# Optimization experiments

Measured on AMD Instinct MI355X. Metric: run time of the kernel, lower is better.

Reference implementation:

```python
import jax, jax.numpy as jnp
import numpy as np

SR = 16000
MAX_Q = 2.0
MIN_D, MAX_D = 0.1, 2.0
MIN_W = 2.0 * np.pi * 20.0 / SR  # 2*pi*20/sr, lowest cutoff in rad/sample
MIN_Q = 0.1
B, T = 32, 65536


def map_logspace(x, lo, hi):
    # log-spaced interpolation: x in [0,1] -> [lo, hi]
    return lo * (hi / lo) ** x


def segment_average(params, seg_ids, num_segments):
    # average params over each onset-delimited segment, broadcast back to [B,T,4]
    def one(p, s):
        sums = jax.ops.segment_sum(p, s, num_segments=num_segments)
        cnt = jax.ops.segment_sum(jnp.ones(s.shape, p.dtype), s, num_segments=num_segments)
        avg = sums / jnp.maximum(cnt, 1.0)[:, None]
        return avg[s]
    return jax.vmap(one)(params, seg_ids)


def pluck_comb(f0, mu, x):
    # Mathematically identical to the scatter-built dense (B,T,D) FIR in the
    # original: y[b,t] = x[b,t] - (1-alfa)*x[b, t-(z+1)] - alfa*x[b, t-(z+2)]
    # (lag k corresponds to coefficient slot k-1; out-of-range lags are zero).
    Tx = x.shape[1]
    p = f0 * mu                       # fractional pluck position in samples
    z = jnp.floor(p)
    alfa = p - z
    zi = z.astype(jnp.int32)
    t = jnp.arange(Tx, dtype=jnp.int32)[None, :]

    def lag(idx):
        g = jnp.take_along_axis(x, jnp.clip(idx, 0, Tx - 1), axis=1)
        return jnp.where(idx >= 0, g, jnp.zeros((), x.dtype))

    return x - (1.0 - alfa) * lag(t - (zi + 1)) - alfa * lag(t - (zi + 2))


def tv_lp_biquad(x, w_mod, q_mod):
    # Time-varying RBJ low-pass biquad, transposed direct-form II, coefficients
    # recomputed per sample from w_mod,q_mod in (0,1).
    w = map_logspace(w_mod, MIN_W, jnp.pi)     # cutoff rad/sample in [min_w, pi]
    q = map_logspace(q_mod, MIN_Q, MAX_Q)      # resonance in [0.1, max_q]
    cw, sw = jnp.cos(w), jnp.sin(w)
    alpha = sw / (2.0 * q)
    a0 = 1.0 + alpha
    b0 = (1.0 - cw) / (2.0 * a0)
    b1 = (1.0 - cw) / a0
    b2 = b0
    a1 = (-2.0 * cw) / a0
    a2 = (1.0 - alpha) / a0

    xs = tuple(jnp.swapaxes(a, 0, 1) for a in (x, b0, b1, b2, a1, a2))  # [T,B]

    def step(carry, inp):
        s1, s2 = carry
        xt, b0t, b1t, b2t, a1t, a2t = inp
        y = b0t * xt + s1
        s1n = b1t * xt - a1t * y + s2
        s2n = b2t * xt - a2t * y
        return (s1n, s2n), y

    Bx = x.shape[0]
    init = (jnp.zeros((Bx,), x.dtype), jnp.zeros((Bx,), x.dtype))
    _, y = jax.lax.scan(step, init, xs)
    return jnp.swapaxes(y, 0, 1)


def _forward(f0, x, params, onsets):
    Tx = x.shape[1]
    # segment ids: cumulative count of onsets along time
    seg_ids = jnp.cumsum(onsets.astype(jnp.int32), axis=1)
    params = segment_average(params, seg_ids, Tx + 1)
    distance = map_logspace(jax.nn.sigmoid(params[..., 0]), MIN_D, MAX_D)
    w_mod = jax.nn.sigmoid(params[..., 1])
    q_mod = jax.nn.sigmoid(params[..., 2])
    mu = jax.nn.sigmoid(params[..., 3])
    xd = x * distance
    xc = pluck_comb(f0, mu, xd)
    return tv_lp_biquad(xc, w_mod, q_mod)


def setup_inputs() -> dict:
    key = jax.random.key(0)
    k1, k2, k3, k4 = jax.random.split(key, 4)
    # f0 is a fundamental period in samples (80-160 Hz at sr=16k)
    f0 = 100.0 + 100.0 * jax.random.uniform(k1, (B, T), jnp.float32)
    x = jax.random.normal(k2, (B, T), jnp.float32)
    params = jax.random.normal(k3, (B, T, 4), jnp.float32)
    onsets = (jax.random.uniform(k4, (B, T)) < 1e-3).astype(jnp.int32)  # sparse note onsets
    return {"f0": f0, "input": x, "params": params, "onsets": onsets}


def reference(f0, input, params, onsets):
    return _forward(f0, input, params, onsets)
```

## Files before the change

### kernel.cpp

```cpp
#include <hip/hip_runtime.h>
#include <cstdint>


namespace {
constexpr int B = 32;
constexpr int T = 65536;
constexpr int MAXSEG = 2048;
constexpr int SB = 2048;
constexpr int HALO = 256;
constexpr int PARTS = T / SB;
constexpr int NB = B * PARTS;

constexpr float MIN_W_C  = 0.00785398163397448279f;
constexpr float LOG2_400 = 8.64385618977472436f;
constexpr float LOG2_20  = 4.32192809488736235f;

__device__ __forceinline__ float sigmoid_precise(float v) {
  return 1.0f / (1.0f + expf(-v));
}
__device__ __forceinline__ int pad16(int i) { return i + (i >> 4); }
}

__global__ void __launch_bounds__(1024) k_segids(
    const int* __restrict__ onsets, unsigned short* __restrict__ seg_ids,
    int* __restrict__ onsetPos, int* __restrict__ nseg) {
  __shared__ int wcnt[16];
  int b = blockIdx.x, tid = threadIdx.x;
  int w = tid >> 6, lane = tid & 63;
  int rb = b * T;
  int sp = w * 4096;
  const int4* po = (const int4*)(onsets + rb + sp);
  int run = 0;
#pragma unroll 4
  for (int it = 0; it < 16; ++it) {
    int4 v = po[it * 64 + lane];
    run += (v.x != 0) + (v.y != 0) + (v.z != 0) + (v.w != 0);
  }
  for (int off = 32; off; off >>= 1) run += __shfl_down(run, off);
  if (lane == 0) wcnt[w] = run;
  __syncthreads();
  int base = 0, tot = 0;
  for (int i = 0; i < 16; ++i) { int c = wcnt[i]; tot += c; if (i < w) base += c; }
  if (tid == 0) nseg[b] = tot;
  unsigned long long bm = (1ull << lane) - 1ull;
  int runp = base;
  for (int it = 0; it < 16; ++it) {
    int tb = sp + it * 256;
    int o0 = onsets[rb + tb + lane];
    int o1 = onsets[rb + tb + 64 + lane];
    int o2 = onsets[rb + tb + 128 + lane];
    int o3 = onsets[rb + tb + 192 + lane];
    int os[4] = {o0 != 0, o1 != 0, o2 != 0, o3 != 0};
#pragma unroll
    for (int j = 0; j < 4; ++j) {
      int t = tb + j * 64 + lane;
      unsigned long long m = __ballot(os[j]);
      int sid = runp + __popcll(m & bm) + os[j];
      seg_ids[rb + t] = (unsigned short)min(sid, MAXSEG - 1);
      if (os[j] && sid <= MAXSEG) onsetPos[b * MAXSEG + sid - 1] = t;
      runp += __popcll(m);
    }
  }
}

__global__ void k_segavg(const float* __restrict__ params, const int* __restrict__ onsetPos,
                         const int* __restrict__ nseg, float4* __restrict__ segc,
                         float* __restrict__ segd) {
  __shared__ float part[4][4];
  int b = blockIdx.x >> 6;
  int s0 = blockIdx.x & 63;
  int tid = threadIdx.x;
  int n = nseg[b];
  const float4* pp = (const float4*)params;
  for (int s = s0; s <= n; s += 64) {
    int start = (s == 0) ? 0 : onsetPos[b * MAXSEG + min(s, MAXSEG) - 1];
    int end   = (s == n) ? T : onsetPos[b * MAXSEG + min(s, MAXSEG - 1)];
    float a0 = 0.f, a1 = 0.f, a2 = 0.f, a3 = 0.f;
    for (int t = start + tid; t < end; t += 256) {
      float4 pv = pp[b * T + t];
      a0 += pv.x; a1 += pv.y; a2 += pv.z; a3 += pv.w;
    }
    for (int off = 32; off; off >>= 1) {
      a0 += __shfl_down(a0, off); a1 += __shfl_down(a1, off);
      a2 += __shfl_down(a2, off); a3 += __shfl_down(a3, off);
    }
    if ((tid & 63) == 0) {
      int w = tid >> 6;
      part[w][0] = a0; part[w][1] = a1; part[w][2] = a2; part[w][3] = a3;
    }
    __syncthreads();
    if (tid == 0) {
      float t0 = 0.f, t1 = 0.f, t2 = 0.f, t3 = 0.f;
      for (int w = 0; w < 4; ++w) {
        t0 += part[w][0]; t1 += part[w][1]; t2 += part[w][2]; t3 += part[w][3];
      }
      float inv = 1.0f / (float)max(end - start, 1);
      float av0 = t0 * inv, av1 = t1 * inv, av2 = t2 * inv, av3 = t3 * inv;
      float dist = 0.1f * exp2f(sigmoid_precise(av0) * LOG2_20);
      float wv   = MIN_W_C * exp2f(sigmoid_precise(av1) * LOG2_400);
      float qv   = 0.1f * exp2f(sigmoid_precise(av2) * LOG2_20);
      float mu   = sigmoid_precise(av3);
      float sw = sinf(wv), cw = cosf(wv);
      float alpha = sw / (2.0f * qv);
      float a0c = 1.0f + alpha;
      float b0 = (1.0f - cw) / (2.0f * a0c);
      float na1 = 2.0f * cw / a0c;
      float na2 = (alpha - 1.0f) / a0c;
      int sl = min(s, MAXSEG - 1);
      segc[b * MAXSEG + sl] = make_float4(mu, b0, na1, na2);
      segd[b * MAXSEG + sl] = dist;
    }
    __syncthreads();
  }
}

__global__ void __launch_bounds__(256) k_compose(
    const float* __restrict__ f0, const float* __restrict__ x,
    const unsigned short* __restrict__ seg, const float4* __restrict__ segc,
    const float* __restrict__ segd, float* __restrict__ p0g,
    float* __restrict__ aggP) {
  __shared__ float s_xd[2448];
  __shared__ float wagg[4][6];
  int tid = threadIdx.x;
  int blk = blockIdx.x;
  int b = blk >> 5, part = blk & (PARTS - 1);
  int rb = b * T, rs = b * MAXSEG, bs = part * SB;

  for (int j = tid; j < SB + HALO; j += 256) {
    int tr = bs - HALO + j;
    float v = 0.f;
    if (tr >= 0) {
      int s = (int)seg[rb + tr];
      v = x[rb + tr] * segd[rs + s];
    }
    s_xd[pad16(j)] = v;
  }
  __syncthreads();

  int lane = tid & 63, w = tid >> 6;
  int t0l = tid * 8;
  const float4* f4 = (const float4*)(f0 + rb + bs + t0l);
  const uint4* sg4 = (const uint4*)(seg + rb + bs + t0l);
  uint4 sv = sg4[0];
  unsigned sw_[4] = {sv.x, sv.y, sv.z, sv.w};
  float p0c[8];
  float A00 = 1.f, A01 = 0.f, A10 = 0.f, A11 = 1.f, d0 = 0.f, d1 = 0.f;
#pragma unroll
  for (int k = 0; k < 2; ++k) {
    float4 fv = f4[k];
    float fs[4] = {fv.x, fv.y, fv.z, fv.w};
#pragma unroll
    for (int q = 0; q < 4; ++q) {
      int idx = k * 4 + q;
      int li = t0l + idx;
      int s = (int)((sw_[idx >> 1] >> (16 * (idx & 1))) & 0xFFFFu);
      float4 sc = segc[rs + s];
      float p = fs[q] * sc.x;
      float z = floorf(p);
      float alfa = p - z;
      int zi = min((int)z, HALO - 8);
      int i1 = li - zi - 1 + HALO;
      float xl1 = s_xd[pad16(i1)];
      float xl2 = s_xd[pad16(i1 - 1)];
      float xc = s_xd[pad16(li + HALO)] - (1.f - alfa) * xl1 - alfa * xl2;
      float p0 = sc.y * xc;
      p0c[idx] = p0;
      float na1 = sc.z, na2 = sc.w;
      float c0v = p0 * (2.f + na1);
      float c1v = p0 * (1.f + na2);
      float nA00 = fmaf(na1, A00, A10);
      float nA01 = fmaf(na1, A01, A11);
      float nd0  = fmaf(na1, d0, d1 + c0v);
      float nA10 = na2 * A00;
      float nA11 = na2 * A01;
      float nd1  = fmaf(na2, d0, c1v);
      A00 = nA00; A01 = nA01; A10 = nA10; A11 = nA11; d0 = nd0; d1 = nd1;
    }
  }
  float4* pp4 = (float4*)(p0g + rb + bs + t0l);
  pp4[0] = make_float4(p0c[0], p0c[1], p0c[2], p0c[3]);
  pp4[1] = make_float4(p0c[4], p0c[5], p0c[6], p0c[7]);
#pragma unroll
  for (int off = 1; off < 64; off <<= 1) {
    float R00 = __shfl_down(A00, off), R01 = __shfl_down(A01, off);
    float R10 = __shfl_down(A10, off), R11 = __shfl_down(A11, off);
    float Rd0 = __shfl_down(d0, off),  Rd1 = __shfl_down(d1, off);
    float n00 = fmaf(R00, A00, R01 * A10);
    float n01 = fmaf(R00, A01, R01 * A11);
    float n10 = fmaf(R10, A00, R11 * A10);
    float n11 = fmaf(R10, A01, R11 * A11);
    float nd0 = fmaf(R00, d0, fmaf(R01, d1, Rd0));
    float nd1 = fmaf(R10, d0, fmaf(R11, d1, Rd1));
    A00 = n00; A01 = n01; A10 = n10; A11 = n11; d0 = nd0; d1 = nd1;
  }
  if (lane == 0) {
    wagg[w][0] = A00; wagg[w][1] = A01; wagg[w][2] = A10;
    wagg[w][3] = A11; wagg[w][4] = d0;  wagg[w][5] = d1;
  }
  __syncthreads();
  if (tid == 0) {
    float G00 = wagg[0][0], G01 = wagg[0][1], G10 = wagg[0][2];
    float G11 = wagg[0][3], Gd0 = wagg[0][4], Gd1 = wagg[0][5];
    for (int i = 1; i < 4; ++i) {
      float W00 = wagg[i][0], W01 = wagg[i][1], W10 = wagg[i][2];
      float W11 = wagg[i][3], Wd0 = wagg[i][4], Wd1 = wagg[i][5];
      float n00 = fmaf(W00, G00, W01 * G10);
      float n01 = fmaf(W00, G01, W01 * G11);
      float n10 = fmaf(W10, G00, W11 * G10);
      float n11 = fmaf(W10, G01, W11 * G11);
      float nd0 = fmaf(W00, Gd0, fmaf(W01, Gd1, Wd0));
      float nd1 = fmaf(W10, Gd0, fmaf(W11, Gd1, Wd1));
      G00 = n00; G01 = n01; G10 = n10; G11 = n11; Gd0 = nd0; Gd1 = nd1;
    }
    float* gp = aggP + blk * 6;
    gp[0] = G00; gp[1] = G01; gp[2] = G10; gp[3] = G11; gp[4] = Gd0; gp[5] = Gd1;
  }
}

__global__ void __launch_bounds__(256) k_apply(
    const float* __restrict__ p0g, const unsigned short* __restrict__ seg,
    const float4* __restrict__ segc, const float* __restrict__ aggP,
    float* __restrict__ out) {
  __shared__ float wagg[4][6];
  __shared__ float rowpref[2];
  int tid = threadIdx.x;
  int blk = blockIdx.x;
  int b = blk >> 5, part = blk & (PARTS - 1);
  int rb = b * T, rs = b * MAXSEG, bs = part * SB;
  int lane = tid & 63, w = tid >> 6;
  int t0l = tid * 8;

  const float4* pp4 = (const float4*)(p0g + rb + bs + t0l);
  const uint4* sg4 = (const uint4*)(seg + rb + bs + t0l);
  uint4 sv = sg4[0];
  unsigned sw_[4] = {sv.x, sv.y, sv.z, sv.w};
  float p0c[8], na1c[8], na2c[8];
  float A00 = 1.f, A01 = 0.f, A10 = 0.f, A11 = 1.f, d0 = 0.f, d1 = 0.f;
#pragma unroll
  for (int k = 0; k < 2; ++k) {
    float4 pv = pp4[k];
    float ps[4] = {pv.x, pv.y, pv.z, pv.w};
#pragma unroll
    for (int q = 0; q < 4; ++q) {
      int idx = k * 4 + q;
      int s = (int)((sw_[idx >> 1] >> (16 * (idx & 1))) & 0xFFFFu);
      float4 sc = segc[rs + s];
      float p0 = ps[q];
      float na1 = sc.z, na2 = sc.w;
      p0c[idx] = p0; na1c[idx] = na1; na2c[idx] = na2;
      float c0v = p0 * (2.f + na1);
      float c1v = p0 * (1.f + na2);
      float nA00 = fmaf(na1, A00, A10);
      float nA01 = fmaf(na1, A01, A11);
      float nd0  = fmaf(na1, d0, d1 + c0v);
      float nA10 = na2 * A00;
      float nA11 = na2 * A01;
      float nd1  = fmaf(na2, d0, c1v);
      A00 = nA00; A01 = nA01; A10 = nA10; A11 = nA11; d0 = nd0; d1 = nd1;
    }
  }
#pragma unroll
  for (int off = 1; off < 64; off <<= 1) {
    float P00 = __shfl_up(A00, off), P01 = __shfl_up(A01, off);
    float P10 = __shfl_up(A10, off), P11 = __shfl_up(A11, off);
    float Pd0 = __shfl_up(d0, off),  Pd1 = __shfl_up(d1, off);
    if (lane >= off) {
      float nA00 = fmaf(A00, P00, A01 * P10);
      float nA01 = fmaf(A00, P01, A01 * P11);
      float nA10 = fmaf(A10, P00, A11 * P10);
      float nA11 = fmaf(A10, P01, A11 * P11);
      float nd0  = fmaf(A00, Pd0, fmaf(A01, Pd1, d0));
      float nd1  = fmaf(A10, Pd0, fmaf(A11, Pd1, d1));
      A00 = nA00; A01 = nA01; A10 = nA10; A11 = nA11; d0 = nd0; d1 = nd1;
    }
  }
  if (lane == 63) {
    wagg[w][0] = A00; wagg[w][1] = A01; wagg[w][2] = A10;
    wagg[w][3] = A11; wagg[w][4] = d0;  wagg[w][5] = d1;
  }
  if (tid == 0) {
    float R00 = 1.f, R01 = 0.f, R10 = 0.f, R11 = 1.f, Rd0 = 0.f, Rd1 = 0.f;
    int base = (blk - part) * 6;
    for (int j = 0; j < part; ++j) {
      const float* gp = aggP + base + j * 6;
      float W00 = gp[0], W01 = gp[1], W10 = gp[2], W11 = gp[3], Wd0 = gp[4], Wd1 = gp[5];
      float n00 = fmaf(W00, R00, W01 * R10);
      float n01 = fmaf(W00, R01, W01 * R11);
      float n10 = fmaf(W10, R00, W11 * R10);
      float n11 = fmaf(W10, R01, W11 * R11);
      float nd0 = fmaf(W00, Rd0, fmaf(W01, Rd1, Wd0));
      float nd1 = fmaf(W10, Rd0, fmaf(W11, Rd1, Wd1));
      R00 = n00; R01 = n01; R10 = n10; R11 = n11; Rd0 = nd0; Rd1 = nd1;
    }
    rowpref[0] = Rd0; rowpref[1] = Rd1;
  }
  __syncthreads();
  float E00 = __shfl_up(A00, 1), E01 = __shfl_up(A01, 1);
  float E10 = __shfl_up(A10, 1), E11 = __shfl_up(A11, 1);
  float Ed0 = __shfl_up(d0, 1),  Ed1 = __shfl_up(d1, 1);
  if (lane == 0) { E00 = 1.f; E01 = 0.f; E10 = 0.f; E11 = 1.f; Ed0 = 0.f; Ed1 = 0.f; }
  float P00 = 1.f, P01 = 0.f, P10 = 0.f, P11 = 1.f, Pd0 = 0.f, Pd1 = 0.f;
  for (int i = 0; i < w; ++i) {
    float W00 = wagg[i][0], W01 = wagg[i][1], W10 = wagg[i][2];
    float W11 = wagg[i][3], Wd0 = wagg[i][4], Wd1 = wagg[i][5];
    float n00 = fmaf(W00, P00, W01 * P10);
    float n01 = fmaf(W00, P01, W01 * P11);
    float n10 = fmaf(W10, P00, W11 * P10);
    float n11 = fmaf(W10, P01, W11 * P11);
    float nd0 = fmaf(W00, Pd0, fmaf(W01, Pd1, Wd0));
    float nd1 = fmaf(W10, Pd0, fmaf(W11, Pd1, Wd1));
    P00 = n00; P01 = n01; P10 = n10; P11 = n11; Pd0 = nd0; Pd1 = nd1;
  }
  float X00 = fmaf(E00, P00, E01 * P10);
  float X01 = fmaf(E00, P01, E01 * P11);
  float X10 = fmaf(E10, P00, E11 * P10);
  float X11 = fmaf(E10, P01, E11 * P11);
  float Xd0 = fmaf(E00, Pd0, fmaf(E01, Pd1, Ed0));
  float Xd1 = fmaf(E10, Pd0, fmaf(E11, Pd1, Ed1));
  float r0 = rowpref[0], r1 = rowpref[1];
  float s1 = fmaf(X00, r0, fmaf(X01, r1, Xd0));
  float s2 = fmaf(X10, r0, fmaf(X11, r1, Xd1));
  float4* o4 = (float4*)(out + rb + bs + t0l);
#pragma unroll
  for (int k = 0; k < 2; ++k) {
    float ys[4];
#pragma unroll
    for (int q = 0; q < 4; ++q) {
      int idx = k * 4 + q;
      float p0 = p0c[idx];
      float y = p0 + s1;
      ys[q] = y;
      float ns1 = fmaf(na1c[idx], y, fmaf(2.f, p0, s2));
      float ns2 = fmaf(na2c[idx], y, p0);
      s1 = ns1; s2 = ns2;
    }
    o4[k] = make_float4(ys[0], ys[1], ys[2], ys[3]);
  }
}

extern "C" void kernel_launch(void* const* d_in, const int* in_sizes, int n_in,
                              void* d_out, int out_size, void* d_ws, size_t ws_size,
                              hipStream_t stream) {
  const float* f0     = (const float*)d_in[0];
  const float* x      = (const float*)d_in[1];
  const float* params = (const float*)d_in[2];
  const int*   onsets = (const int*)d_in[3];
  float* out = (float*)d_out;

  char* w = (char*)d_ws;
  auto alloc = [&](size_t bytes) -> void* {
    void* p = (void*)w;
    w += (bytes + 255) & ~(size_t)255;
    return p;
  };
  unsigned short* seg_ids = (unsigned short*)alloc(sizeof(unsigned short) * B * T);
  int*    onsetPos = (int*)alloc(sizeof(int) * B * MAXSEG);
  int*    nseg     = (int*)alloc(sizeof(int) * B);
  float4* segc     = (float4*)alloc(sizeof(float4) * B * MAXSEG);
  float*  segd     = (float*)alloc(sizeof(float) * B * MAXSEG);
  float*  p0g      = (float*)alloc(sizeof(float) * B * T);
  float*  aggP     = (float*)alloc(sizeof(float) * 6 * NB);
  (void)in_sizes; (void)n_in; (void)out_size; (void)ws_size;

  k_segids <<<B, 1024, 0, stream>>>(onsets, seg_ids, onsetPos, nseg);
  k_segavg <<<B * 64, 256, 0, stream>>>(params, onsetPos, nseg, segc, segd);
  k_compose<<<NB, 256, 0, stream>>>(f0, x, seg_ids, segc, segd, p0g, aggP);
  k_apply  <<<NB, 256, 0, stream>>>(p0g, seg_ids, segc, aggP, out);
}
```

Measured before the change: 130.5 us.

## Split segment-id scan into count and scan kernels across more waves

Replaces the single per-batch 1024-thread segment-id kernel (32 blocks) with two kernels: a count kernel where each of 64 waves per batch row counts onsets in its span, and a scan kernel that computes exclusive prefixes across waves with shuffles before writing segment ids and onset positions. The aim is to spread the scan over 512 blocks so more of the GPU is busy in this stage. The cost is an extra kernel launch and a second read of the onsets array, and the scan loop now issues one scalar load per iteration instead of four.

```diff
diff --git a/kernel.cpp b/kernel.cpp
--- a/kernel.cpp
+++ b/kernel.cpp
@@ -6,6 +6,8 @@
 constexpr int B = 32;
 constexpr int T = 65536;
 constexpr int MAXSEG = 2048;
+constexpr int WV = 64;
+constexpr int SPAN = T / WV;
 constexpr int SB = 2048;
 constexpr int HALO = 256;
 constexpr int PARTS = T / SB;
@@ -21,45 +23,45 @@
 __device__ __forceinline__ int pad16(int i) { return i + (i >> 4); }
 }
 
-__global__ void __launch_bounds__(1024) k_segids(
-    const int* __restrict__ onsets, unsigned short* __restrict__ seg_ids,
-    int* __restrict__ onsetPos, int* __restrict__ nseg) {
-  __shared__ int wcnt[16];
-  int b = blockIdx.x, tid = threadIdx.x;
-  int w = tid >> 6, lane = tid & 63;
-  int rb = b * T;
-  int sp = w * 4096;
-  const int4* po = (const int4*)(onsets + rb + sp);
+__global__ void k_count(const int* __restrict__ onsets, int* __restrict__ cnt) {
+  int gw = (blockIdx.x * blockDim.x + threadIdx.x) >> 6;
+  int lane = threadIdx.x & 63;
+  int b = gw / WV, wv = gw % WV;
+  const int4* po = (const int4*)(onsets + b * T + wv * SPAN);
   int run = 0;
-#pragma unroll 4
-  for (int it = 0; it < 16; ++it) {
+  for (int it = 0; it < SPAN / 256; ++it) {
     int4 v = po[it * 64 + lane];
     run += (v.x != 0) + (v.y != 0) + (v.z != 0) + (v.w != 0);
   }
   for (int off = 32; off; off >>= 1) run += __shfl_down(run, off);
-  if (lane == 0) wcnt[w] = run;
-  __syncthreads();
-  int base = 0, tot = 0;
-  for (int i = 0; i < 16; ++i) { int c = wcnt[i]; tot += c; if (i < w) base += c; }
-  if (tid == 0) nseg[b] = tot;
+  if (lane == 0) cnt[b * WV + wv] = run;
+}
+
+__global__ void k_segids(const int* __restrict__ onsets, const int* __restrict__ cnt,
+                         unsigned short* __restrict__ seg_ids, int* __restrict__ onsetPos,
+                         int* __restrict__ nseg) {
+  int gw = (blockIdx.x * blockDim.x + threadIdx.x) >> 6;
+  int lane = threadIdx.x & 63;
+  int b = gw / WV, wv = gw % WV;
+  const int rb = b * T;
+  int t0 = wv * SPAN;
+  int cl = (lane < wv) ? cnt[b * WV + lane] : 0;
+  int ct = cnt[b * WV + lane];
+  for (int off = 1; off < 64; off <<= 1) {
+    cl += __shfl_xor(cl, off);
+    ct += __shfl_xor(ct, off);
+  }
+  if (wv == 0 && lane == 0) nseg[b] = ct;
+  int run = cl;
   unsigned long long bm = (1ull << lane) - 1ull;
-  int runp = base;
-  for (int it = 0; it < 16; ++it) {
-    int tb = sp + it * 256;
-    int o0 = onsets[rb + tb + lane];
-    int o1 = onsets[rb + tb + 64 + lane];
-    int o2 = onsets[rb + tb + 128 + lane];
-    int o3 = onsets[rb + tb + 192 + lane];
-    int os[4] = {o0 != 0, o1 != 0, o2 != 0, o3 != 0};
-#pragma unroll
-    for (int j = 0; j < 4; ++j) {
-      int t = tb + j * 64 + lane;
-      unsigned long long m = __ballot(os[j]);
-      int sid = runp + __popcll(m & bm) + os[j];
-      seg_ids[rb + t] = (unsigned short)min(sid, MAXSEG - 1);
-      if (os[j] && sid <= MAXSEG) onsetPos[b * MAXSEG + sid - 1] = t;
-      runp += __popcll(m);
-    }
+  for (int it = 0; it < SPAN / 64; ++it) {
+    int t = t0 + it * 64 + lane;
+    int o = onsets[rb + t] != 0;
+    unsigned long long m = __ballot(o);
+    int sid = run + __popcll(m & bm) + o;
+    seg_ids[rb + t] = (unsigned short)min(sid, MAXSEG - 1);
+    if (o && sid <= MAXSEG) onsetPos[b * MAXSEG + sid - 1] = t;
+    run += __popcll(m);
   }
 }
 
@@ -354,6 +356,7 @@
     return p;
   };
   unsigned short* seg_ids = (unsigned short*)alloc(sizeof(unsigned short) * B * T);
+  int*    cnt      = (int*)alloc(sizeof(int) * B * WV);
   int*    onsetPos = (int*)alloc(sizeof(int) * B * MAXSEG);
   int*    nseg     = (int*)alloc(sizeof(int) * B);
   float4* segc     = (float4*)alloc(sizeof(float4) * B * MAXSEG);
@@ -362,7 +365,8 @@
   float*  aggP     = (float*)alloc(sizeof(float) * 6 * NB);
   (void)in_sizes; (void)n_in; (void)out_size; (void)ws_size;
 
-  k_segids <<<B, 1024, 0, stream>>>(onsets, seg_ids, onsetPos, nseg);
+  k_count  <<<512, 256, 0, stream>>>(onsets, cnt);
+  k_segids <<<512, 256, 0, stream>>>(onsets, cnt, seg_ids, onsetPos, nseg);
   k_segavg <<<B * 64, 256, 0, stream>>>(params, onsetPos, nseg, segc, segd);
   k_compose<<<NB, 256, 0, stream>>>(f0, x, seg_ids, segc, segd, p0g, aggP);
   k_apply  <<<NB, 256, 0, stream>>>(p0g, seg_ids, segc, aggP, out);
```

Result: no change. 129.1 us (median of 2 runs) (-1.1%).
